# Performance work log

Hardware: AMD Instinct MI355X
Metric: run time of the kernel (lower is better)

## Reference

```python
import jax, jax.numpy as jnp
import numpy as np

DIM = 1024
NUM_HEADS = 16
HEAD_DIM = DIM // NUM_HEADS


def setup_inputs() -> dict:
    key = jax.random.key(0)
    ks = jax.random.split(key, 9)
    s = 1.0 / np.sqrt(DIM)
    x = jax.random.normal(ks[0], (2, 2048, DIM), dtype=jnp.float32)
    Wq = jax.random.normal(ks[1], (DIM, DIM), dtype=jnp.float32) * s
    bq = jax.random.normal(ks[2], (DIM,), dtype=jnp.float32) * s
    Wk = jax.random.normal(ks[3], (DIM, DIM), dtype=jnp.float32) * s
    bk = jax.random.normal(ks[4], (DIM,), dtype=jnp.float32) * s
    Wv = jax.random.normal(ks[5], (DIM, DIM), dtype=jnp.float32) * s
    bv = jax.random.normal(ks[6], (DIM,), dtype=jnp.float32) * s
    Wo = jax.random.normal(ks[7], (DIM, DIM), dtype=jnp.float32) * s
    bo = jax.random.normal(ks[8], (DIM,), dtype=jnp.float32) * s
    return {"x": x, "Wq": Wq, "bq": bq, "Wk": Wk, "bk": bk,
            "Wv": Wv, "bv": bv, "Wo": Wo, "bo": bo}


def _softmax_one(x, axis=-1):
    # softmax with +1 in the denominator (quiet attention)
    x = x - jnp.max(x, axis=axis, keepdims=True)
    ex = jnp.exp(x)
    return ex / (1.0 + jnp.sum(ex, axis=axis, keepdims=True))


def reference(x, Wq, bq, Wk, bk, Wv, bv, Wo, bo):
    B, L, D = x.shape
    H, hd = NUM_HEADS, HEAD_DIM
    q = (x @ Wq + bq).reshape(B, L, H, hd).transpose(0, 2, 1, 3)  # b h l d
    k = (x @ Wk + bk).reshape(B, L, H, hd).transpose(0, 2, 1, 3)
    v = (x @ Wv + bv).reshape(B, L, H, hd).transpose(0, 2, 1, 3)
    scores = jnp.einsum('bhqd,bhkd->bhqk', q, k) / np.sqrt(hd).astype(np.float32)
    # causal additive mask: -inf above the diagonal (matches torch generate_square_subsequent_mask)
    causal = jnp.triu(jnp.full((L, L), -jnp.inf, dtype=scores.dtype), k=1)
    scores = scores + causal
    attn = _softmax_one(scores, axis=-1)
    ctx = jnp.einsum('bhqk,bhkd->bhqd', attn, v)
    ctx = ctx.transpose(0, 2, 1, 3).reshape(B, L, D)
    return ctx @ Wo + bo
```

## Files before the change

kernel.cpp:

```cpp
#include <hip/hip_runtime.h>
#include <hip/hip_bf16.h>
#include <cstdint>
#include <cstddef>

#define DIMN 1024
#define NHEAD 16
#define HDIM 64
#define NB 2
#define SEQ 2048
#define MROWS 4096
#define BHN 32
#define QKV_STRIDE 4194304
#define BH_ELEMS 131072

typedef float f32x4 __attribute__((ext_vector_type(4)));
typedef __bf16 bf16x8 __attribute__((ext_vector_type(8)));

__device__ __forceinline__ void async_copy16(const void* g, void* l) {
    __builtin_amdgcn_global_load_lds(
        (__attribute__((address_space(1))) void*)(g),
        (__attribute__((address_space(3))) void*)(l), 16, 0, 0);
}

__device__ __forceinline__ unsigned short bf16_bits(float f) {
    __hip_bfloat16 hb = __float2bfloat16(f);
    return *(unsigned short*)&hb;
}

__global__ __launch_bounds__(256) void prep_kernel(
        const float* __restrict__ x, const float* __restrict__ bq,
        const float* __restrict__ bk, const float* __restrict__ bv,
        const float* __restrict__ Wq, const float* __restrict__ Wk,
        const float* __restrict__ Wv, const float* __restrict__ Wo,
        __hip_bfloat16* __restrict__ xbf, float* __restrict__ biasq,
        __hip_bfloat16* __restrict__ wqkvt, __hip_bfloat16* __restrict__ wot) {
    __shared__ float tile[32][33];
    const int bid = blockIdx.x;
    const int t = threadIdx.x;
    if (bid < 4096) {
        int i = (bid * 256 + t) * 4;
        float4 v = *(const float4*)(x + i);
        xbf[i + 0] = __float2bfloat16(v.x);
        xbf[i + 1] = __float2bfloat16(v.y);
        xbf[i + 2] = __float2bfloat16(v.z);
        xbf[i + 3] = __float2bfloat16(v.w);
    } else if (bid < 4099) {
        int base = (bid - 4096) * 1024 + t * 4;
#pragma unroll
        for (int e = 0; e < 4; e++) {
            int gi = base + e;
            int which = gi >> 10, off = gi & 1023;
            float v = (which == 0) ? bq[off] : (which == 1) ? bk[off] : bv[off];
            biasq[gi] = v;
        }
    } else {
        int rr = bid - 4099;
        int z = rr >> 10;
        int tid = rr & 1023;
        int n0 = (tid & 31) * 32, k0 = (tid >> 5) * 32;
        const float* in = (z == 0) ? Wq : (z == 1) ? Wk : (z == 2) ? Wv : Wo;
        __hip_bfloat16* out = (z == 3) ? wot : wqkvt + (size_t)z * DIMN * DIMN;
        int tx = t & 31, ty = t >> 5;
#pragma unroll
        for (int r = 0; r < 32; r += 8)
            tile[ty + r][tx] = in[(size_t)(k0 + ty + r) * DIMN + n0 + tx];
        __syncthreads();
#pragma unroll
        for (int r = 0; r < 32; r += 8)
            out[(size_t)(n0 + ty + r) * DIMN + k0 + tx] =
                __float2bfloat16(tile[tx][ty + r]);
    }
}

__global__ __launch_bounds__(256) void gemm_qkv_kernel(
        const __hip_bfloat16* __restrict__ A, const __hip_bfloat16* __restrict__ Bt,
        const float* __restrict__ bias, __hip_bfloat16* __restrict__ qkv,
        __hip_bfloat16* __restrict__ vt) {
    __shared__ __align__(16) unsigned short As[128 * 32];
    __shared__ __align__(16) unsigned short Bs[128 * 32];
    const int t = threadIdx.x;
    const int m0 = blockIdx.y * 128;
    const int n0 = blockIdx.x * 128;
    const int lane = t & 63;
    const int w = t >> 6;
    const int wm = (w >> 1) * 64;
    const int wn = (w & 1) * 64;
    const int r16 = lane & 15;
    const int quad = lane >> 4;

    f32x4 acc[4][4];
#pragma unroll
    for (int i = 0; i < 4; i++)
#pragma unroll
        for (int j = 0; j < 4; j++) acc[i][j] = (f32x4){0.f, 0.f, 0.f, 0.f};

    const int rowA = t >> 2;
    const int kch = (t & 3) * 8;

    for (int k0 = 0; k0 < DIMN; k0 += 32) {
        __syncthreads();
#pragma unroll
        for (int r = 0; r < 2; r++) {
            int row = rowA + r * 64;
            async_copy16(A + (size_t)(m0 + row) * DIMN + k0 + kch,
                         (char*)As + (size_t)(row * 4 + (t & 3)) * 16);
            async_copy16(Bt + (size_t)(n0 + row) * DIMN + k0 + kch,
                         (char*)Bs + (size_t)(row * 4 + (t & 3)) * 16);
        }
        __syncthreads();

        bf16x8 af[4], bfr[4];
#pragma unroll
        for (int i = 0; i < 4; i++)
            af[i] = *(const bf16x8*)&As[(wm + i * 16 + r16) * 32 + quad * 8];
#pragma unroll
        for (int j = 0; j < 4; j++)
            bfr[j] = *(const bf16x8*)&Bs[(wn + j * 16 + r16) * 32 + quad * 8];
#pragma unroll
        for (int i = 0; i < 4; i++)
#pragma unroll
            for (int j = 0; j < 4; j++)
                acc[i][j] = __builtin_amdgcn_mfma_f32_16x16x32_bf16(
                    af[i], bfr[j], acc[i][j], 0, 0, 0);
    }

#pragma unroll
    for (int i = 0; i < 4; i++)
#pragma unroll
        for (int j = 0; j < 4; j++) {
            int n = n0 + wn + j * 16 + r16;
            float bv = bias[n];
            int which = n >> 10, rem = n & 1023;
            int h = rem >> 6, d = rem & 63;
            int mbase = m0 + wm + i * 16 + quad * 4;
            int b = mbase >> 11;
            int lrow = mbase & 2047;
            int bh = b * NHEAD + h;
            if (which == 2) {
                ushort4 pk;
                pk.x = bf16_bits(acc[i][j][0] + bv);
                pk.y = bf16_bits(acc[i][j][1] + bv);
                pk.z = bf16_bits(acc[i][j][2] + bv);
                pk.w = bf16_bits(acc[i][j][3] + bv);
                *(ushort4*)(vt + (size_t)bh * BH_ELEMS + (size_t)d * SEQ + lrow) = pk;
            } else {
#pragma unroll
                for (int r = 0; r < 4; r++) {
                    float v = acc[i][j][r] + bv;
                    if (which == 0) v *= 0.125f;
                    qkv[(size_t)which * QKV_STRIDE + (size_t)bh * BH_ELEMS +
                        (size_t)(lrow + r) * 64 + d] = __float2bfloat16(v);
                }
            }
        }
}

__global__ __launch_bounds__(256) void gemm_out_kernel(
        const __hip_bfloat16* __restrict__ A, const __hip_bfloat16* __restrict__ Bt,
        const float* __restrict__ bias, float* __restrict__ outp) {
    __shared__ __align__(16) unsigned short As[64 * 32];
    __shared__ __align__(16) unsigned short Bs[128 * 32];
    const int t = threadIdx.x;
    const int m0 = blockIdx.y * 64;
    const int n0 = blockIdx.x * 128;
    const int lane = t & 63;
    const int w = t >> 6;
    const int wm = (w >> 1) * 32;
    const int wn = (w & 1) * 64;
    const int r16 = lane & 15;
    const int quad = lane >> 4;

    f32x4 acc[2][4];
#pragma unroll
    for (int i = 0; i < 2; i++)
#pragma unroll
        for (int j = 0; j < 4; j++) acc[i][j] = (f32x4){0.f, 0.f, 0.f, 0.f};

    const int rowA = t >> 2;
    const int kch = (t & 3) * 8;

    for (int k0 = 0; k0 < DIMN; k0 += 32) {
        __syncthreads();
        async_copy16(A + (size_t)(m0 + rowA) * DIMN + k0 + kch, (char*)As + t * 16);
#pragma unroll
        for (int r = 0; r < 2; r++) {
            int row = rowA + r * 64;
            async_copy16(Bt + (size_t)(n0 + row) * DIMN + k0 + kch,
                         (char*)Bs + (size_t)(row * 4 + (t & 3)) * 16);
        }
        __syncthreads();

        bf16x8 af[2], bfr[4];
#pragma unroll
        for (int i = 0; i < 2; i++)
            af[i] = *(const bf16x8*)&As[(wm + i * 16 + r16) * 32 + quad * 8];
#pragma unroll
        for (int j = 0; j < 4; j++)
            bfr[j] = *(const bf16x8*)&Bs[(wn + j * 16 + r16) * 32 + quad * 8];
#pragma unroll
        for (int i = 0; i < 2; i++)
#pragma unroll
            for (int j = 0; j < 4; j++)
                acc[i][j] = __builtin_amdgcn_mfma_f32_16x16x32_bf16(
                    af[i], bfr[j], acc[i][j], 0, 0, 0);
    }

#pragma unroll
    for (int i = 0; i < 2; i++)
#pragma unroll
        for (int j = 0; j < 4; j++) {
            int n = n0 + wn + j * 16 + r16;
            float bv = bias[n];
#pragma unroll
            for (int r = 0; r < 4; r++) {
                int m = m0 + wm + i * 16 + quad * 4 + r;
                outp[(size_t)m * DIMN + n] = acc[i][j][r] + bv;
            }
        }
}

__global__ __launch_bounds__(512, 4) void attn_mfma_kernel(
        const __hip_bfloat16* __restrict__ qkv, const __hip_bfloat16* __restrict__ vt,
        __hip_bfloat16* __restrict__ ctxout) {
    __shared__ __align__(16) unsigned short SMEM[28672];

    const int bx = blockIdx.x;
    const int g = bx >> 5;
    const int qt = (g < 8) ? 15 - g : g - 8;
    const int bh = bx & 31;
    const int t = threadIdx.x;
    const int lane = t & 63;
    const int w = t >> 6;
    const int half = w >> 2;
    const int wq = w & 3;
    const int r16 = lane & 15;
    const int quad = lane >> 4;
    const int qbase = qt * 128 + wq * 32;
    const int swz = quad ^ ((r16 >> 1) & 3);
    const int pkey = (r16 >> 1) & 3;

    const __hip_bfloat16* Qg = qkv + (size_t)bh * BH_ELEMS;
    const __hip_bfloat16* Kg = qkv + (size_t)QKV_STRIDE + (size_t)bh * BH_ELEMS;
    const __hip_bfloat16* Vtg = vt + (size_t)bh * BH_ELEMS;

    unsigned short* PsW = SMEM + 24576 + w * 512;

    const int cb_kp = (t & 511) >> 8;
    const int cb_rr = ((t & 511) >> 2) & 63;
    const int cb_cg = ((t & 511) & 3) ^ ((cb_rr >> 1) & 3);

    bf16x8 bq[2][2];
#pragma unroll
    for (int ng = 0; ng < 2; ng++)
#pragma unroll
        for (int kp = 0; kp < 2; kp++)
            bq[ng][kp] = *(const bf16x8*)(Qg + (size_t)(qbase + ng * 16 + r16) * 64 +
                                          kp * 32 + quad * 8);

    f32x4 oT[4][2];
#pragma unroll
    for (int mt = 0; mt < 4; mt++)
#pragma unroll
        for (int ng = 0; ng < 2; ng++) oT[mt][ng] = (f32x4){0.f, 0.f, 0.f, 0.f};
    float m_run[2] = {-1e30f, -1e30f};
    float z_run[2] = {0.f, 0.f};

    const int niter = qt + 1;

#pragma unroll
    for (int it = 0; it < 2; it++) {
        int cl = it * 512 + t;
        int ktile = (cl >> 9) ? (qt + 1) : 0;
        async_copy16(Kg + (size_t)(ktile * 64 + cb_rr) * 64 + cb_kp * 32 + cb_cg * 8,
                     (char*)SMEM + (size_t)cl * 16);
    }

#pragma unroll 1
    for (int i = 0; i < niter; i++) {
        const int curb = i & 1;
        __syncthreads();

#pragma unroll
        for (int it = 0; it < 2; it++) {
            int cl = it * 512 + t;
            int ktile = (cl >> 9) ? (qt + 1 + i) : i;
            async_copy16(Vtg + (size_t)cb_rr * SEQ + ktile * 64 + cb_kp * 32 + cb_cg * 8,
                         (char*)SMEM + 32768 + (size_t)cl * 16);
        }
        if (i + 1 < niter) {
            int ktA = i + 1;
            int ktB = qt + 2 + i; if (ktB > 31) ktB = 31;
#pragma unroll
            for (int it = 0; it < 2; it++) {
                int cl = it * 512 + t;
                int ktile = (cl >> 9) ? ktB : ktA;
                async_copy16(Kg + (size_t)(ktile * 64 + cb_rr) * 64 + cb_kp * 32 + cb_cg * 8,
                             (char*)SMEM + (size_t)(curb ^ 1) * 16384 + (size_t)cl * 16);
            }
        }

        const int ktile = half ? (qt + 1 + i) : i;
        const bool active = (ktile * 64 <= qbase + 31);

        f32x4 st[4][2];
        if (active) {
            const unsigned short* KsW = SMEM + curb * 8192 + half * 4096;
#pragma unroll
            for (int mt = 0; mt < 4; mt++)
#pragma unroll
                for (int ng = 0; ng < 2; ng++) st[mt][ng] = (f32x4){0.f, 0.f, 0.f, 0.f};
#pragma unroll
            for (int mt = 0; mt < 4; mt++)
#pragma unroll
                for (int kp = 0; kp < 2; kp++) {
                    bf16x8 ak = *(const bf16x8*)&KsW[kp * 2048 + (mt * 16 + r16) * 32 + swz * 8];
                    st[mt][0] = __builtin_amdgcn_mfma_f32_16x16x32_bf16(ak, bq[0][kp], st[mt][0], 0, 0, 0);
                    st[mt][1] = __builtin_amdgcn_mfma_f32_16x16x32_bf16(ak, bq[1][kp], st[mt][1], 0, 0, 0);
                }

            if (ktile * 64 + 63 > qbase) {
#pragma unroll
                for (int mt = 0; mt < 4; mt++) {
                    int kb = ktile * 64 + mt * 16 + quad * 4;
#pragma unroll
                    for (int ng = 0; ng < 2; ng++) {
                        int q = qbase + ng * 16 + r16;
#pragma unroll
                        for (int r = 0; r < 4; r++)
                            if (kb + r > q) st[mt][ng][r] = -__builtin_inff();
                    }
                }
            }

#pragma unroll
            for (int mt = 0; mt < 4; mt++)
#pragma unroll
                for (int ng = 0; ng < 2; ng++) {
                    float s0 = st[mt][ng][0], s1 = st[mt][ng][1];
                    float s2 = st[mt][ng][2], s3 = st[mt][ng][3];
                    m_run[ng] = fmaxf(m_run[ng], fmaxf(fmaxf(s0, s1), fmaxf(s2, s3)));
                    float p0 = __expf(s0), p1 = __expf(s1);
                    float p2 = __expf(s2), p3 = __expf(s3);
                    z_run[ng] += (p0 + p1) + (p2 + p3);
                    st[mt][ng][0] = p0; st[mt][ng][1] = p1;
                    st[mt][ng][2] = p2; st[mt][ng][3] = p3;
                }
        }
        __syncthreads();

        if (active) {
            const unsigned short* VsW = SMEM + 16384 + half * 4096;
#pragma unroll
            for (int p = 0; p < 2; p++) {
#pragma unroll
                for (int ng = 0; ng < 2; ng++) {
#pragma unroll
                    for (int ml = 0; ml < 2; ml++) {
                        int mt = p * 2 + ml;
                        ushort4 pk;
                        pk.x = bf16_bits(st[mt][ng][0]);
                        pk.y = bf16_bits(st[mt][ng][1]);
                        pk.z = bf16_bits(st[mt][ng][2]);
                        pk.w = bf16_bits(st[mt][ng][3]);
                        int c = (ml * 2 + (quad >> 1)) ^ pkey;
                        *(ushort4*)&PsW[r16 * 32 + c * 8 + (quad & 1) * 4] = pk;
                    }
                    bf16x8 bp = *(const bf16x8*)&PsW[r16 * 32 + (quad ^ pkey) * 8];
#pragma unroll
                    for (int mt = 0; mt < 4; mt++) {
                        bf16x8 av = *(const bf16x8*)&VsW[p * 2048 + (mt * 16 + r16) * 32 + swz * 8];
                        oT[mt][ng] = __builtin_amdgcn_mfma_f32_16x16x32_bf16(
                            av, bp, oT[mt][ng], 0, 0, 0);
                    }
                }
            }
        }
    }

#pragma unroll
    for (int off = 16; off < 64; off <<= 1)
#pragma unroll
        for (int ng = 0; ng < 2; ng++) {
            m_run[ng] = fmaxf(m_run[ng], __shfl_xor(m_run[ng], off, 64));
            z_run[ng] += __shfl_xor(z_run[ng], off, 64);
        }

    __syncthreads();
    f32x4* CbO = (f32x4*)SMEM;
    f32x4* Ml = (f32x4*)((char*)SMEM + 32768);
    if (w >= 4) {
        int w4 = w - 4;
#pragma unroll
        for (int mt = 0; mt < 4; mt++)
#pragma unroll
            for (int ng = 0; ng < 2; ng++)
                CbO[((w4 * 8 + mt * 2 + ng) << 6) + lane] = oT[mt][ng];
        f32x4 ml;
        ml[0] = m_run[0]; ml[1] = m_run[1]; ml[2] = z_run[0]; ml[3] = z_run[1];
        Ml[(w4 << 6) + lane] = ml;
    }
    __syncthreads();
    if (w < 4) {
        f32x4 ml = Ml[(w << 6) + lane];
        float rd[2];
#pragma unroll
        for (int ng = 0; ng < 2; ng++) {
            float mtot = fmaxf(m_run[ng], ml[ng]);
            float ztot = z_run[ng] + ml[2 + ng];
            rd[ng] = 1.f / (__expf(mtot) + ztot);
        }
        const int b = bh >> 4, h = bh & 15;
#pragma unroll
        for (int mt = 0; mt < 4; mt++)
#pragma unroll
            for (int ng = 0; ng < 2; ng++) {
                f32x4 O1 = CbO[((w * 8 + mt * 2 + ng) << 6) + lane];
                int q = qbase + ng * 16 + r16;
                ushort4 pk;
                pk.x = bf16_bits((oT[mt][ng][0] + O1[0]) * rd[ng]);
                pk.y = bf16_bits((oT[mt][ng][1] + O1[1]) * rd[ng]);
                pk.z = bf16_bits((oT[mt][ng][2] + O1[2]) * rd[ng]);
                pk.w = bf16_bits((oT[mt][ng][3] + O1[3]) * rd[ng]);
                *(ushort4*)(ctxout + ((size_t)(b * SEQ + q)) * DIMN + h * 64 +
                            mt * 16 + quad * 4) = pk;
            }
    }
}


extern "C" void kernel_launch(void* const* d_in, const int* in_sizes, int n_in,
                              void* d_out, int out_size, void* d_ws, size_t ws_size,
                              hipStream_t stream) {
    const float* x  = (const float*)d_in[0];
    const float* Wq = (const float*)d_in[1];
    const float* bq = (const float*)d_in[2];
    const float* Wk = (const float*)d_in[3];
    const float* bk = (const float*)d_in[4];
    const float* Wv = (const float*)d_in[5];
    const float* bv = (const float*)d_in[6];
    const float* Wo = (const float*)d_in[7];
    const float* bo = (const float*)d_in[8];

    char* ws = (char*)d_ws;
    __hip_bfloat16* xbf   = (__hip_bfloat16*)(ws);
    __hip_bfloat16* wqkvt = (__hip_bfloat16*)(ws + (8u << 20));
    __hip_bfloat16* wot   = (__hip_bfloat16*)(ws + (14u << 20));
    float*          biasq = (float*)(ws + (16u << 20));
    __hip_bfloat16* qkv   = (__hip_bfloat16*)(ws + (16u << 20) + 65536u);
    __hip_bfloat16* vt    = (__hip_bfloat16*)(ws + (16u << 20) + 65536u + (16u << 20));
    __hip_bfloat16* ctx   = (__hip_bfloat16*)(ws + (16u << 20) + 65536u + (24u << 20));
    float* out = (float*)d_out;

    prep_kernel<<<8195, 256, 0, stream>>>(x, bq, bk, bv, Wq, Wk, Wv, Wo,
                                          xbf, biasq, wqkvt, wot);
    gemm_qkv_kernel<<<dim3(24, 32), 256, 0, stream>>>(xbf, wqkvt, biasq, qkv, vt);
    attn_mfma_kernel<<<512, 512, 0, stream>>>(qkv, vt, ctx);
    gemm_out_kernel<<<dim3(8, 64), 256, 0, stream>>>(ctx, wot, bo, out);
}
```

Baseline: 178.8 us.

## Double GEMM K-tile to 64 with XOR-swizzled LDS and exp2 softmax

Both GEMM kernels now load 64-wide K slices per iteration instead of 32, halving the number of barrier pairs. The LDS layout uses an XOR swizzle on the 16-byte chunks to avoid bank conflicts on the fragment reads. The attention softmax switches from __expf to exp2f by folding log2(e) into the Q scale, which saves a multiply per exponential. Shared memory per block doubles, which may lower occupancy.

```diff
diff --git a/kernel.cpp b/kernel.cpp
--- a/kernel.cpp
+++ b/kernel.cpp
@@ -12,6 +12,8 @@
 #define BHN 32
 #define QKV_STRIDE 4194304
 #define BH_ELEMS 131072
+
+#define QSCALE 0.18033688011112042f
 
 typedef float f32x4 __attribute__((ext_vector_type(4)));
 typedef __bf16 bf16x8 __attribute__((ext_vector_type(8)));
@@ -76,8 +78,8 @@
         const __hip_bfloat16* __restrict__ A, const __hip_bfloat16* __restrict__ Bt,
         const float* __restrict__ bias, __hip_bfloat16* __restrict__ qkv,
         __hip_bfloat16* __restrict__ vt) {
-    __shared__ __align__(16) unsigned short As[128 * 32];
-    __shared__ __align__(16) unsigned short Bs[128 * 32];
+    __shared__ __align__(16) unsigned short As[128 * 64];
+    __shared__ __align__(16) unsigned short Bs[128 * 64];
     const int t = threadIdx.x;
     const int m0 = blockIdx.y * 128;
     const int n0 = blockIdx.x * 128;
@@ -94,34 +96,44 @@
 #pragma unroll
         for (int j = 0; j < 4; j++) acc[i][j] = (f32x4){0.f, 0.f, 0.f, 0.f};
 
-    const int rowA = t >> 2;
-    const int kch = (t & 3) * 8;
-
-    for (int k0 = 0; k0 < DIMN; k0 += 32) {
-        __syncthreads();
-#pragma unroll
-        for (int r = 0; r < 2; r++) {
-            int row = rowA + r * 64;
-            async_copy16(A + (size_t)(m0 + row) * DIMN + k0 + kch,
-                         (char*)As + (size_t)(row * 4 + (t & 3)) * 16);
-            async_copy16(Bt + (size_t)(n0 + row) * DIMN + k0 + kch,
-                         (char*)Bs + (size_t)(row * 4 + (t & 3)) * 16);
-        }
-        __syncthreads();
-
-        bf16x8 af[4], bfr[4];
-#pragma unroll
-        for (int i = 0; i < 4; i++)
-            af[i] = *(const bf16x8*)&As[(wm + i * 16 + r16) * 32 + quad * 8];
-#pragma unroll
-        for (int j = 0; j < 4; j++)
-            bfr[j] = *(const bf16x8*)&Bs[(wn + j * 16 + r16) * 32 + quad * 8];
-#pragma unroll
-        for (int i = 0; i < 4; i++)
-#pragma unroll
-            for (int j = 0; j < 4; j++)
-                acc[i][j] = __builtin_amdgcn_mfma_f32_16x16x32_bf16(
-                    af[i], bfr[j], acc[i][j], 0, 0, 0);
+    const int rowS = t >> 3;
+    const int kcS  = t & 7;
+
+    for (int k0 = 0; k0 < DIMN; k0 += 64) {
+        __syncthreads();
+#pragma unroll
+        for (int r = 0; r < 4; r++) {
+            int row = rowS + r * 32;
+            int kc = kcS ^ (row & 7);
+            async_copy16(A + (size_t)(m0 + row) * DIMN + k0 + kc * 8,
+                         (char*)As + (size_t)(row * 8 + kcS) * 16);
+            async_copy16(Bt + (size_t)(n0 + row) * DIMN + k0 + kc * 8,
+                         (char*)Bs + (size_t)(row * 8 + kcS) * 16);
+        }
+        __syncthreads();
+
+#pragma unroll
+        for (int kp = 0; kp < 2; kp++) {
+            bf16x8 af[4], bfr[4];
+#pragma unroll
+            for (int i = 0; i < 4; i++) {
+                int row = wm + i * 16 + r16;
+                int slot = (kp * 4 + quad) ^ (row & 7);
+                af[i] = *(const bf16x8*)&As[row * 64 + slot * 8];
+            }
+#pragma unroll
+            for (int j = 0; j < 4; j++) {
+                int row = wn + j * 16 + r16;
+                int slot = (kp * 4 + quad) ^ (row & 7);
+                bfr[j] = *(const bf16x8*)&Bs[row * 64 + slot * 8];
+            }
+#pragma unroll
+            for (int i = 0; i < 4; i++)
+#pragma unroll
+                for (int j = 0; j < 4; j++)
+                    acc[i][j] = __builtin_amdgcn_mfma_f32_16x16x32_bf16(
+                        af[i], bfr[j], acc[i][j], 0, 0, 0);
+        }
     }
 
 #pragma unroll
@@ -147,7 +159,7 @@
 #pragma unroll
                 for (int r = 0; r < 4; r++) {
                     float v = acc[i][j][r] + bv;
-                    if (which == 0) v *= 0.125f;
+                    if (which == 0) v *= QSCALE;
                     qkv[(size_t)which * QKV_STRIDE + (size_t)bh * BH_ELEMS +
                         (size_t)(lrow + r) * 64 + d] = __float2bfloat16(v);
                 }
@@ -158,8 +170,8 @@
 __global__ __launch_bounds__(256) void gemm_out_kernel(
         const __hip_bfloat16* __restrict__ A, const __hip_bfloat16* __restrict__ Bt,
         const float* __restrict__ bias, float* __restrict__ outp) {
-    __shared__ __align__(16) unsigned short As[64 * 32];
-    __shared__ __align__(16) unsigned short Bs[128 * 32];
+    __shared__ __align__(16) unsigned short As[64 * 64];
+    __shared__ __align__(16) unsigned short Bs[128 * 64];
     const int t = threadIdx.x;
     const int m0 = blockIdx.y * 64;
     const int n0 = blockIdx.x * 128;
@@ -176,33 +188,49 @@
 #pragma unroll
         for (int j = 0; j < 4; j++) acc[i][j] = (f32x4){0.f, 0.f, 0.f, 0.f};
 
-    const int rowA = t >> 2;
-    const int kch = (t & 3) * 8;
-
-    for (int k0 = 0; k0 < DIMN; k0 += 32) {
-        __syncthreads();
-        async_copy16(A + (size_t)(m0 + rowA) * DIMN + k0 + kch, (char*)As + t * 16);
+    const int rowS = t >> 3;
+    const int kcS  = t & 7;
+
+    for (int k0 = 0; k0 < DIMN; k0 += 64) {
+        __syncthreads();
 #pragma unroll
         for (int r = 0; r < 2; r++) {
-            int row = rowA + r * 64;
-            async_copy16(Bt + (size_t)(n0 + row) * DIMN + k0 + kch,
-                         (char*)Bs + (size_t)(row * 4 + (t & 3)) * 16);
-        }
-        __syncthreads();
-
-        bf16x8 af[2], bfr[4];
-#pragma unroll
-        for (int i = 0; i < 2; i++)
-            af[i] = *(const bf16x8*)&As[(wm + i * 16 + r16) * 32 + quad * 8];
-#pragma unroll
-        for (int j = 0; j < 4; j++)
-            bfr[j] = *(const bf16x8*)&Bs[(wn + j * 16 + r16) * 32 + quad * 8];
-#pragma unroll
-        for (int i = 0; i < 2; i++)
-#pragma unroll
-            for (int j = 0; j < 4; j++)
-                acc[i][j] = __builtin_amdgcn_mfma_f32_16x16x32_bf16(
-                    af[i], bfr[j], acc[i][j], 0, 0, 0);
+            int row = rowS + r * 32;
+            int kc = kcS ^ (row & 7);
+            async_copy16(A + (size_t)(m0 + row) * DIMN + k0 + kc * 8,
+                         (char*)As + (size_t)(row * 8 + kcS) * 16);
+        }
+#pragma unroll
+        for (int r = 0; r < 4; r++) {
+            int row = rowS + r * 32;
+            int kc = kcS ^ (row & 7);
+            async_copy16(Bt + (size_t)(n0 + row) * DIMN + k0 + kc * 8,
+                         (char*)Bs + (size_t)(row * 8 + kcS) * 16);
+        }
+        __syncthreads();
+
+#pragma unroll
+        for (int kp = 0; kp < 2; kp++) {
+            bf16x8 af[2], bfr[4];
+#pragma unroll
+            for (int i = 0; i < 2; i++) {
+                int row = wm + i * 16 + r16;
+                int slot = (kp * 4 + quad) ^ (row & 7);
+                af[i] = *(const bf16x8*)&As[row * 64 + slot * 8];
+            }
+#pragma unroll
+            for (int j = 0; j < 4; j++) {
+                int row = wn + j * 16 + r16;
+                int slot = (kp * 4 + quad) ^ (row & 7);
+                bfr[j] = *(const bf16x8*)&Bs[row * 64 + slot * 8];
+            }
+#pragma unroll
+            for (int i = 0; i < 2; i++)
+#pragma unroll
+                for (int j = 0; j < 4; j++)
+                    acc[i][j] = __builtin_amdgcn_mfma_f32_16x16x32_bf16(
+                        af[i], bfr[j], acc[i][j], 0, 0, 0);
+        }
     }
 
 #pragma unroll
@@ -339,8 +367,8 @@
                     float s0 = st[mt][ng][0], s1 = st[mt][ng][1];
                     float s2 = st[mt][ng][2], s3 = st[mt][ng][3];
                     m_run[ng] = fmaxf(m_run[ng], fmaxf(fmaxf(s0, s1), fmaxf(s2, s3)));
-                    float p0 = __expf(s0), p1 = __expf(s1);
-                    float p2 = __expf(s2), p3 = __expf(s3);
+                    float p0 = exp2f(s0), p1 = exp2f(s1);
+                    float p2 = exp2f(s2), p3 = exp2f(s3);
                     z_run[ng] += (p0 + p1) + (p2 + p3);
                     st[mt][ng][0] = p0; st[mt][ng][1] = p1;
                     st[mt][ng][2] = p2; st[mt][ng][3] = p3;
@@ -407,7 +435,7 @@
         for (int ng = 0; ng < 2; ng++) {
             float mtot = fmaxf(m_run[ng], ml[ng]);
             float ztot = z_run[ng] + ml[2 + ng];
-            rd[ng] = 1.f / (__expf(mtot) + ztot);
+            rd[ng] = 1.f / (exp2f(mtot) + ztot);
         }
         const int b = bh >> 4, h = bh & 15;
 #pragma unroll
```

After: 190.9 us. +6.8%, slower.

## Rewrite QKV GEMM as 256x256 triple-buffered pipeline and use exp2 softmax

Applied to the files above, without the earlier changes.

The QKV projection GEMM moves to 256x256 tiles with 512 threads and a three-stage async LDS ring buffer using swizzled layout. Loads for tile k+2 are issued while the current tile's MFMAs run, with s_setprio around the compute. This is meant to hide global-load latency and cut LDS bank conflicts and per-iteration syncs. Separately, Q is pre-scaled by log2(e)/8 so the attention softmax can use exp2f instead of __expf. The trade-off is a grid of only 192 blocks at one block per CU, which may underfill the GPU.

```diff
diff --git a/kernel.cpp b/kernel.cpp
--- a/kernel.cpp
+++ b/kernel.cpp
@@ -12,6 +12,8 @@
 #define BHN 32
 #define QKV_STRIDE 4194304
 #define BH_ELEMS 131072
+
+#define QSCALE 0.18033688011112042f
 
 typedef float f32x4 __attribute__((ext_vector_type(4)));
 typedef __bf16 bf16x8 __attribute__((ext_vector_type(8)));
@@ -72,70 +74,117 @@
     }
 }
 
-__global__ __launch_bounds__(256) void gemm_qkv_kernel(
+__global__ __launch_bounds__(512, 1) void gemm_qkv_kernel(
         const __hip_bfloat16* __restrict__ A, const __hip_bfloat16* __restrict__ Bt,
         const float* __restrict__ bias, __hip_bfloat16* __restrict__ qkv,
         __hip_bfloat16* __restrict__ vt) {
-    __shared__ __align__(16) unsigned short As[128 * 32];
-    __shared__ __align__(16) unsigned short Bs[128 * 32];
+    __shared__ __align__(16) unsigned short SM[49152];
     const int t = threadIdx.x;
-    const int m0 = blockIdx.y * 128;
-    const int n0 = blockIdx.x * 128;
+    const int m0 = blockIdx.y * 256;
+    const int n0 = blockIdx.x * 256;
     const int lane = t & 63;
     const int w = t >> 6;
-    const int wm = (w >> 1) * 64;
-    const int wn = (w & 1) * 64;
+    const int wmid = w >> 2;
+    const int wnid = w & 3;
     const int r16 = lane & 15;
     const int quad = lane >> 4;
-
-    f32x4 acc[4][4];
-#pragma unroll
-    for (int i = 0; i < 4; i++)
+    const int rsw = (quad ^ ((r16 >> 1) & 3)) * 8;
+    const int blr0 = (wnid & 1) * 64;
+
+    const int srow = t >> 2;
+    const int scsw = (t & 3) ^ ((srow >> 1) & 3);
+    const __hip_bfloat16* Ag = A + (size_t)(m0 + srow) * DIMN + scsw * 8;
+    const __hip_bfloat16* Bg = Bt + (size_t)(n0 + srow) * DIMN + scsw * 8;
+
+    f32x4 acc[8][4];
+#pragma unroll
+    for (int i = 0; i < 8; i++)
 #pragma unroll
         for (int j = 0; j < 4; j++) acc[i][j] = (f32x4){0.f, 0.f, 0.f, 0.f};
 
-    const int rowA = t >> 2;
-    const int kch = (t & 3) * 8;
-
-    for (int k0 = 0; k0 < DIMN; k0 += 32) {
-        __syncthreads();
-#pragma unroll
-        for (int r = 0; r < 2; r++) {
-            int row = rowA + r * 64;
-            async_copy16(A + (size_t)(m0 + row) * DIMN + k0 + kch,
-                         (char*)As + (size_t)(row * 4 + (t & 3)) * 16);
-            async_copy16(Bt + (size_t)(n0 + row) * DIMN + k0 + kch,
-                         (char*)Bs + (size_t)(row * 4 + (t & 3)) * 16);
-        }
-        __syncthreads();
+#pragma unroll
+    for (int tt = 0; tt < 2; tt++) {
+#pragma unroll
+        for (int h = 0; h < 2; h++)
+            async_copy16(Ag + (size_t)h * 131072 + tt * 32,
+                         (char*)(SM + (tt * 2 + h) * 4096 + t * 8));
+#pragma unroll
+        for (int h = 0; h < 2; h++)
+            async_copy16(Bg + (size_t)h * 131072 + tt * 32,
+                         (char*)(SM + 24576 + (tt * 2 + h) * 4096 + t * 8));
+    }
+
+    int sl = 0;
+#pragma unroll 1
+    for (int tt = 0; tt < 32; ++tt) {
+        const int sl2 = (sl >= 1) ? (sl - 1) : 2;
+        if (tt == 31) {
+            asm volatile("s_waitcnt vmcnt(0)" ::: "memory");
+        } else {
+            asm volatile("s_waitcnt vmcnt(4)" ::: "memory");
+        }
+        __builtin_amdgcn_s_barrier();
+
+        const unsigned short* Asl = SM + (sl * 2 + wmid) * 4096;
+        const unsigned short* Bsl = SM + 24576 + (sl * 2 + (wnid >> 1)) * 4096;
 
         bf16x8 af[4], bfr[4];
 #pragma unroll
         for (int i = 0; i < 4; i++)
-            af[i] = *(const bf16x8*)&As[(wm + i * 16 + r16) * 32 + quad * 8];
+            af[i] = *(const bf16x8*)&Asl[(i * 16 + r16) * 32 + rsw];
 #pragma unroll
         for (int j = 0; j < 4; j++)
-            bfr[j] = *(const bf16x8*)&Bs[(wn + j * 16 + r16) * 32 + quad * 8];
+            bfr[j] = *(const bf16x8*)&Bsl[(blr0 + j * 16 + r16) * 32 + rsw];
+        if (tt < 30) {
+#pragma unroll
+            for (int h = 0; h < 2; h++)
+                async_copy16(Ag + (size_t)h * 131072 + (tt + 2) * 32,
+                             (char*)(SM + (sl2 * 2 + h) * 4096 + t * 8));
+        }
+        __builtin_amdgcn_s_setprio(1);
 #pragma unroll
         for (int i = 0; i < 4; i++)
 #pragma unroll
             for (int j = 0; j < 4; j++)
                 acc[i][j] = __builtin_amdgcn_mfma_f32_16x16x32_bf16(
                     af[i], bfr[j], acc[i][j], 0, 0, 0);
-    }
-
-#pragma unroll
-    for (int i = 0; i < 4; i++)
-#pragma unroll
-        for (int j = 0; j < 4; j++) {
-            int n = n0 + wn + j * 16 + r16;
-            float bv = bias[n];
-            int which = n >> 10, rem = n & 1023;
-            int h = rem >> 6, d = rem & 63;
-            int mbase = m0 + wm + i * 16 + quad * 4;
-            int b = mbase >> 11;
-            int lrow = mbase & 2047;
-            int bh = b * NHEAD + h;
+        __builtin_amdgcn_s_setprio(0);
+
+        __builtin_amdgcn_s_barrier();
+#pragma unroll
+        for (int i = 0; i < 4; i++)
+            af[i] = *(const bf16x8*)&Asl[((i + 4) * 16 + r16) * 32 + rsw];
+        if (tt < 30) {
+#pragma unroll
+            for (int h = 0; h < 2; h++)
+                async_copy16(Bg + (size_t)h * 131072 + (tt + 2) * 32,
+                             (char*)(SM + 24576 + (sl2 * 2 + h) * 4096 + t * 8));
+        }
+        __builtin_amdgcn_s_setprio(1);
+#pragma unroll
+        for (int i = 0; i < 4; i++)
+#pragma unroll
+            for (int j = 0; j < 4; j++)
+                acc[i + 4][j] = __builtin_amdgcn_mfma_f32_16x16x32_bf16(
+                    af[i], bfr[j], acc[i + 4][j], 0, 0, 0);
+        __builtin_amdgcn_s_setprio(0);
+
+        sl = (sl < 2) ? (sl + 1) : 0;
+    }
+
+    const int which = n0 >> 10;
+#pragma unroll
+    for (int j = 0; j < 4; j++) {
+        const int n = n0 + wnid * 64 + j * 16 + r16;
+        const float bv = bias[n];
+        const int rem = n & 1023;
+        const int h = rem >> 6, d = rem & 63;
+#pragma unroll
+        for (int i = 0; i < 8; i++) {
+            const int mbase = m0 + wmid * 128 + i * 16 + quad * 4;
+            const int b = mbase >> 11;
+            const int lrow = mbase & 2047;
+            const int bh = b * NHEAD + h;
             if (which == 2) {
                 ushort4 pk;
                 pk.x = bf16_bits(acc[i][j][0] + bv);
@@ -147,12 +196,13 @@
 #pragma unroll
                 for (int r = 0; r < 4; r++) {
                     float v = acc[i][j][r] + bv;
-                    if (which == 0) v *= 0.125f;
+                    if (which == 0) v *= QSCALE;
                     qkv[(size_t)which * QKV_STRIDE + (size_t)bh * BH_ELEMS +
                         (size_t)(lrow + r) * 64 + d] = __float2bfloat16(v);
                 }
             }
         }
+    }
 }
 
 __global__ __launch_bounds__(256) void gemm_out_kernel(
@@ -339,8 +389,8 @@
                     float s0 = st[mt][ng][0], s1 = st[mt][ng][1];
                     float s2 = st[mt][ng][2], s3 = st[mt][ng][3];
                     m_run[ng] = fmaxf(m_run[ng], fmaxf(fmaxf(s0, s1), fmaxf(s2, s3)));
-                    float p0 = __expf(s0), p1 = __expf(s1);
-                    float p2 = __expf(s2), p3 = __expf(s3);
+                    float p0 = exp2f(s0), p1 = exp2f(s1);
+                    float p2 = exp2f(s2), p3 = exp2f(s3);
                     z_run[ng] += (p0 + p1) + (p2 + p3);
                     st[mt][ng][0] = p0; st[mt][ng][1] = p1;
                     st[mt][ng][2] = p2; st[mt][ng][3] = p3;
@@ -407,7 +457,7 @@
         for (int ng = 0; ng < 2; ng++) {
             float mtot = fmaxf(m_run[ng], ml[ng]);
             float ztot = z_run[ng] + ml[2 + ng];
-            rd[ng] = 1.f / (__expf(mtot) + ztot);
+            rd[ng] = 1.f / (exp2f(mtot) + ztot);
         }
         const int b = bh >> 4, h = bh & 15;
 #pragma unroll
@@ -453,7 +503,7 @@
 
     prep_kernel<<<8195, 256, 0, stream>>>(x, bq, bk, bv, Wq, Wk, Wv, Wo,
                                           xbf, biasq, wqkvt, wot);
-    gemm_qkv_kernel<<<dim3(24, 32), 256, 0, stream>>>(xbf, wqkvt, biasq, qkv, vt);
+    gemm_qkv_kernel<<<dim3(12, 16), 512, 0, stream>>>(xbf, wqkvt, biasq, qkv, vt);
     attn_mfma_kernel<<<512, 512, 0, stream>>>(qkv, vt, ctx);
     gemm_out_kernel<<<dim3(8, 64), 256, 0, stream>>>(ctx, wot, bo, out);
 }
```

New measurement: 185.1 us. +3.5%, slower.
